# Performance work log

Measured on AMD Instinct MI355X. Metric: run time of the kernel, lower is better.

## Reference

```python
import jax, jax.numpy as jnp
import numpy as np

# Config matching init_kwargs (single TP rank: local heads == total heads)
HID = 1024
NH = 16      # query heads
NKV = 4      # kv heads (GQA)
HD = 64      # head_dim
B = 2
S = 2048
SCALE = 1.0 / HD ** 0.5


def setup_inputs() -> dict:
    key = jax.random.key(0)
    k1, k2, k3 = jax.random.split(key, 3)
    qkv_out = (NH + 2 * NKV) * HD  # 1536
    return {
        "hidden_states": jax.random.normal(k1, (B, S, HID), dtype=jnp.float32),
        "W_qkv": jax.random.normal(k2, (HID, qkv_out), dtype=jnp.float32) * 0.02,
        "W_o": jax.random.normal(k3, (HID, HID), dtype=jnp.float32) * 0.02,
    }


def reference(hidden_states, W_qkv, W_o):
    b, s, _ = hidden_states.shape
    rep = NH // NKV  # GQA repeat factor (repeat_interleave: q head h uses kv group h // rep)

    qkv = hidden_states @ W_qkv  # [B, S, (NH+2*NKV)*HD]
    q, k, v = jnp.split(qkv, [NH * HD, (NH + NKV) * HD], axis=-1)

    # [B, heads, S, HD]
    q = q.reshape(b, s, NH, HD).transpose(0, 2, 1, 3)
    k = k.reshape(b, s, NKV, HD).transpose(0, 2, 1, 3)
    v = v.reshape(b, s, NKV, HD).transpose(0, 2, 1, 3)

    # Group query heads by shared kv head instead of repeat_interleaving K/V in memory.
    qg = q.reshape(b, NKV, rep, s, HD)  # head h = g*rep + r  <=>  kv group g = h // rep
    scores = jnp.einsum("bgrqd,bgkd->bgrqk", qg, k) * SCALE  # [B, NKV, rep, S, S]

    # Causal mask (prefill path: kv_cache is None, seq_len > 1)
    causal = jnp.triu(jnp.ones((s, s), dtype=bool), k=1)
    scores = jnp.where(causal, jnp.finfo(scores.dtype).min, scores)

    attn = jax.nn.softmax(scores, axis=-1)
    out = jnp.einsum("bgrqk,bgkd->bgrqd", attn, v)  # [B, NKV, rep, S, HD]
    out = out.reshape(b, NH, s, HD).transpose(0, 2, 1, 3).reshape(b, s, NH * HD)
    return out @ W_o  # [B, S, HID]
```

## Files before the change

### kernel.cpp

```cpp
#include <hip/hip_runtime.h>
#include <stdint.h>

using u16 = unsigned short;
using u32 = unsigned int;

typedef __attribute__((ext_vector_type(8))) short short8;
typedef __attribute__((ext_vector_type(4))) float f32x4;
typedef __attribute__((ext_vector_type(16))) float f32x16;

__device__ __forceinline__ u16 f2bf(float f) {
  u32 u = __builtin_bit_cast(u32, f);
  u = (u + 0x7fffu + ((u >> 16) & 1u)) >> 16;
  return (u16)u;
}

__device__ __forceinline__ u32 cvtpk(float lo, float hi) {
  u32 r;
  asm("v_cvt_pk_bf16_f32 %0, %1, %2" : "=v"(r) : "v"(lo), "v"(hi));
  return r;
}

__device__ __forceinline__ short8 ld16(const u16* p) {
  uint4 v = *(const uint4*)p;
  union { uint4 u; short8 s; } c; c.u = v; return c.s;
}

__device__ __forceinline__ void gload_lds16(const void* g, void* l) {
  __builtin_amdgcn_global_load_lds(
      (const __attribute__((address_space(1))) void*)g,
      (__attribute__((address_space(3))) void*)l, 16, 0, 0);
}

__device__ __forceinline__ f32x16 mfma32(short8 a, short8 b, f32x16 c) {
  return __builtin_amdgcn_mfma_f32_32x32x16_bf16(a, b, c, 0, 0, 0);
}

__global__ __launch_bounds__(256) void k_prep(const float* __restrict__ hs,
                                              const float* __restrict__ wqkv,
                                              const float* __restrict__ wo,
                                              u16* __restrict__ hsb,
                                              u16* __restrict__ wqkvT,
                                              u16* __restrict__ woT) {
  __shared__ float tile[32][33];
  const int bid = blockIdx.x;
  if (bid < 4096) {
    int i = bid * 256 + threadIdx.x;
    float4 v = ((const float4*)hs)[i];
    ushort4 o;
    o.x = f2bf(v.x); o.y = f2bf(v.y); o.z = f2bf(v.z); o.w = f2bf(v.w);
    ((ushort4*)hsb)[i] = o;
    return;
  }
  const float* in; u16* out; int R, C, bx, by;
  if (bid < 5632) {
    int idx = bid - 4096;
    in = wqkv; out = wqkvT; R = 1024; C = 1536;
    bx = idx % 48; by = idx / 48;
  } else {
    int idx = bid - 5632;
    in = wo; out = woT; R = 1024; C = 1024;
    bx = idx & 31; by = idx >> 5;
  }
  int c0 = bx * 32, r0 = by * 32;
  int tx = threadIdx.x & 31, ty = threadIdx.x >> 5;
#pragma unroll
  for (int i = 0; i < 4; ++i) {
    int r = ty + 8 * i;
    tile[r][tx] = in[(size_t)(r0 + r) * C + c0 + tx];
  }
  __syncthreads();
#pragma unroll
  for (int i = 0; i < 4; ++i) {
    int r = ty + 8 * i;
    out[(size_t)(c0 + r) * R + r0 + tx] = f2bf(tile[tx][r]);
  }
}

__global__ __launch_bounds__(256, 3) void k_gemm_qkv(
    const u16* __restrict__ A, const u16* __restrict__ BT,
    u16* __restrict__ qb, u16* __restrict__ kb, u16* __restrict__ vbT) {
  const int K = 1024;
  __shared__ __align__(16) u16 As[2][64 * 64];
  __shared__ __align__(16) u16 Bs[2][128 * 64];
  const int t = threadIdx.x;
  const int l = t & 63;
  const int wid = t >> 6;
  const int wr = wid >> 1, wc = wid & 1;
  const int lr = l & 15, lg = l >> 4;
  const int cpx = (int)gridDim.x >> 3;
  const int nb = (blockIdx.x & 7) * cpx + ((int)blockIdx.x >> 3);
  const int mt = nb / 12, nt = nb % 12;
  const int m0 = mt << 6, n0 = nt << 7;

  f32x4 zero = {0.f, 0.f, 0.f, 0.f};
  f32x4 acc[2][4];
#pragma unroll
  for (int i = 0; i < 2; ++i)
#pragma unroll
    for (int j = 0; j < 4; ++j) acc[i][j] = zero;

  const u16* Ab = A + (size_t)m0 * K;
  const u16* Bb = BT + (size_t)n0 * K;

  auto STAGE = [&](int kt, int bsel) {
    const u16* Ak = Ab + kt * 64;
    const u16* Bk = Bb + kt * 64;
#pragma unroll
    for (int i = 0; i < 2; ++i) {
      int o16 = i * 256 + t;
      int row = o16 >> 3, c = o16 & 7;
      int sc = c ^ (row & 7);
      gload_lds16(Ak + (size_t)row * K + sc * 8, &As[bsel][o16 * 8]);
    }
#pragma unroll
    for (int i = 0; i < 4; ++i) {
      int o16 = i * 256 + t;
      int row = o16 >> 3, c = o16 & 7;
      int sc = c ^ (row & 7);
      gload_lds16(Bk + (size_t)row * K + sc * 8, &Bs[bsel][o16 * 8]);
    }
  };

  STAGE(0, 0);
  asm volatile("s_waitcnt vmcnt(0)" ::: "memory");
  __builtin_amdgcn_s_barrier();

  for (int kt = 0; kt < 16; ++kt) {
    const int cur = kt & 1;
    if (kt + 1 < 16) STAGE(kt + 1, cur ^ 1);
#pragma unroll
    for (int ks = 0; ks < 2; ++ks) {
      short8 a[2], b[4];
#pragma unroll
      for (int mi = 0; mi < 2; ++mi) {
        int row = wr * 32 + mi * 16 + lr;
        int c = (ks * 4 + lg) ^ (row & 7);
        a[mi] = ld16(&As[cur][(row * 8 + c) * 8]);
      }
#pragma unroll
      for (int ni = 0; ni < 4; ++ni) {
        int row = wc * 64 + ni * 16 + lr;
        int c = (ks * 4 + lg) ^ (row & 7);
        b[ni] = ld16(&Bs[cur][(row * 8 + c) * 8]);
      }
#pragma unroll
      for (int mi = 0; mi < 2; ++mi)
#pragma unroll
        for (int ni = 0; ni < 4; ++ni)
          acc[mi][ni] = __builtin_amdgcn_mfma_f32_16x16x32_bf16(a[mi], b[ni], acc[mi][ni], 0, 0, 0);
    }
    asm volatile("s_waitcnt vmcnt(0)" ::: "memory");
    __builtin_amdgcn_s_barrier();
    asm volatile("" ::: "memory");
  }

#pragma unroll
  for (int mi = 0; mi < 2; ++mi) {
#pragma unroll
    for (int ni = 0; ni < 4; ++ni) {
#pragma unroll
      for (int r = 0; r < 4; ++r) {
        float v = acc[mi][ni][r];
        int m = m0 + wr * 32 + mi * 16 + 4 * lg + r;
        int n = n0 + wc * 64 + ni * 16 + lr;
        int bb = m >> 11, s = m & 2047;
        int tau = s >> 5, i32e = s & 31;
        if (n < 1024) {
          int h = n >> 6, d = n & 63;
          int kc = d >> 4, hi2 = (d >> 3) & 1, e = d & 7;
          qb[((size_t)(bb * 16 + h)) * 131072 +
             (size_t)((tau * 4 + kc) * 64 + (hi2 << 5 | i32e)) * 8 + e] = f2bf(v * 0.18033688f);
        } else if (n < 1280) {
          int g = (n - 1024) >> 6, d = n & 63;
          int kc = d >> 4, hi2 = (d >> 3) & 1, e = d & 7;
          kb[((size_t)(bb * 4 + g)) * 131072 +
             (size_t)((tau * 4 + kc) * 64 + (hi2 << 5 | i32e)) * 8 + e] = f2bf(v);
        } else {
          int g = (n - 1280) >> 6, dT = n & 63;
          int c = (s >> 4) & 1, hi2 = (s >> 3) & 1, e = s & 7;
          int dd = dT >> 5, i32v = dT & 31;
          vbT[((size_t)(bb * 4 + g)) * 131072 +
              (size_t)(((tau * 2 + dd) * 2 + c) * 64 + (hi2 << 5 | i32v)) * 8 + e] = f2bf(v);
        }
      }
    }
  }
}

__global__ __launch_bounds__(256, 2) void k_gemm_out(
    const u16* __restrict__ A, const u16* __restrict__ BT, float* __restrict__ out) {
  const int K = 1024, N = 1024;
  __shared__ __align__(16) u16 As[2][64 * 64];
  __shared__ __align__(16) u16 Bs[2][128 * 64];
  const int t = threadIdx.x;
  const int l = t & 63;
  const int wid = t >> 6;
  const int wr = wid >> 1, wc = wid & 1;
  const int lr = l & 15, lg = l >> 4;
  const int cpx = (int)gridDim.x >> 3;
  const int nb = (blockIdx.x & 7) * cpx + ((int)blockIdx.x >> 3);
  const int mt = nb >> 3, nt = nb & 7;
  const int m0 = mt << 6, n0 = nt << 7;

  f32x4 zero = {0.f, 0.f, 0.f, 0.f};
  f32x4 acc[2][4];
#pragma unroll
  for (int i = 0; i < 2; ++i)
#pragma unroll
    for (int j = 0; j < 4; ++j) acc[i][j] = zero;

  const u16* Ab = A + (size_t)m0 * K;
  const u16* Bb = BT + (size_t)n0 * K;

  auto STAGE = [&](int kt, int bsel) {
    const u16* Ak = Ab + kt * 64;
    const u16* Bk = Bb + kt * 64;
#pragma unroll
    for (int i = 0; i < 2; ++i) {
      int o16 = i * 256 + t;
      int row = o16 >> 3, c = o16 & 7;
      int sc = c ^ (row & 7);
      gload_lds16(Ak + (size_t)row * K + sc * 8, &As[bsel][o16 * 8]);
    }
#pragma unroll
    for (int i = 0; i < 4; ++i) {
      int o16 = i * 256 + t;
      int row = o16 >> 3, c = o16 & 7;
      int sc = c ^ (row & 7);
      gload_lds16(Bk + (size_t)row * K + sc * 8, &Bs[bsel][o16 * 8]);
    }
  };

  STAGE(0, 0);
  asm volatile("s_waitcnt vmcnt(0)" ::: "memory");
  __builtin_amdgcn_s_barrier();

  for (int kt = 0; kt < 16; ++kt) {
    const int cur = kt & 1;
    if (kt + 1 < 16) STAGE(kt + 1, cur ^ 1);
#pragma unroll
    for (int ks = 0; ks < 2; ++ks) {
      short8 a[2], b[4];
#pragma unroll
      for (int mi = 0; mi < 2; ++mi) {
        int row = wr * 32 + mi * 16 + lr;
        int c = (ks * 4 + lg) ^ (row & 7);
        a[mi] = ld16(&As[cur][(row * 8 + c) * 8]);
      }
#pragma unroll
      for (int ni = 0; ni < 4; ++ni) {
        int row = wc * 64 + ni * 16 + lr;
        int c = (ks * 4 + lg) ^ (row & 7);
        b[ni] = ld16(&Bs[cur][(row * 8 + c) * 8]);
      }
#pragma unroll
      for (int mi = 0; mi < 2; ++mi)
#pragma unroll
        for (int ni = 0; ni < 4; ++ni)
          acc[mi][ni] = __builtin_amdgcn_mfma_f32_16x16x32_bf16(a[mi], b[ni], acc[mi][ni], 0, 0, 0);
    }
    asm volatile("s_waitcnt vmcnt(0)" ::: "memory");
    __builtin_amdgcn_s_barrier();
    asm volatile("" ::: "memory");
  }

#pragma unroll
  for (int mi = 0; mi < 2; ++mi)
#pragma unroll
    for (int ni = 0; ni < 4; ++ni)
#pragma unroll
      for (int r = 0; r < 4; ++r) {
        int m = m0 + wr * 32 + mi * 16 + 4 * lg + r;
        int n = n0 + wc * 64 + ni * 16 + lr;
        out[(size_t)m * N + n] = acc[mi][ni][r];
      }
}

__global__ __launch_bounds__(256, 1) void k_attn(const u16* __restrict__ qbuf,
                                                 const u16* __restrict__ kbuf,
                                                 const u16* __restrict__ vbuf,
                                                 u16* __restrict__ attn) {
  __shared__ float osh[2][4096];
  __shared__ float lsh[2][128];
  const int t = threadIdx.x;
  const int l = t & 63, wid = t >> 6;
  const int i32 = l & 31, hi = l >> 5;
  const int bh = blockIdx.x >> 3;
  const int jj = blockIdx.x & 7;
  const int b = bh >> 4, h = bh & 15, g = h >> 2;
  const int slot = wid >> 1, w01 = wid & 1;
  const int cc = jj + slot * 8;
  const int pA = cc, pB = 31 - cc;
  const int split = 16 - cc;

  const u16* qp = qbuf + ((size_t)(b * 16 + h)) * 131072;
  const u16* kp = kbuf + ((size_t)(b * 4 + g)) * 131072;
  const u16* vp = vbuf + ((size_t)(b * 4 + g)) * 131072;

  f32x16 z16 = {0.f, 0.f, 0.f, 0.f, 0.f, 0.f, 0.f, 0.f,
                0.f, 0.f, 0.f, 0.f, 0.f, 0.f, 0.f, 0.f};
  short8 qfa[4], qfb[4];
  f32x16 oa[2], ob[2];
  float la, lb;
  short8 kA[2][4], kB[2][4];

  auto LOADQ = [&](int p) {
#pragma unroll
    for (int kc = 0; kc < 4; ++kc) {
      qfa[kc] = ld16(qp + ((size_t)((2 * p) * 4 + kc) * 64 + l) * 8);
      qfb[kc] = ld16(qp + ((size_t)((2 * p + 1) * 4 + kc) * 64 + l) * 8);
    }
  };

  auto LOADK = [&](short8(&kf)[2][4], int kv0) {
#pragma unroll
    for (int mf = 0; mf < 2; ++mf)
#pragma unroll
      for (int kc = 0; kc < 4; ++kc)
        kf[mf][kc] = ld16(kp + ((size_t)((((kv0 >> 5) + mf) * 4 + kc)) * 64 + l) * 8);
  };

  auto SOFTPV = [&](f32x16(&sc)[2], short8(&vf)[2][2][2], f32x16(&o)[2], float& ls,
                    bool dmask, int ilocb) {
    if (dmask) {
#pragma unroll
      for (int mf = 0; mf < 2; ++mf)
#pragma unroll
        for (int R = 0; R < 16; ++R) {
          int j2 = 32 * mf + (R & 3) + 8 * (R >> 2) + 4 * hi;
          if (j2 > ilocb + i32) sc[mf][R] = -1e30f;
        }
    }
    float s0 = 0.f, s1 = 0.f, s2 = 0.f, s3 = 0.f;
#pragma unroll
    for (int mf = 0; mf < 2; ++mf)
#pragma unroll
      for (int R = 0; R < 16; R += 4) {
        float p0 = __builtin_amdgcn_exp2f(sc[mf][R]);
        float p1 = __builtin_amdgcn_exp2f(sc[mf][R + 1]);
        float p2 = __builtin_amdgcn_exp2f(sc[mf][R + 2]);
        float p3 = __builtin_amdgcn_exp2f(sc[mf][R + 3]);
        sc[mf][R] = p0; sc[mf][R + 1] = p1; sc[mf][R + 2] = p2; sc[mf][R + 3] = p3;
        s0 += p0; s1 += p1; s2 += p2; s3 += p3;
      }
    ls += (s0 + s1) + (s2 + s3);
    short8 pb[2][2];
#pragma unroll
    for (int mf = 0; mf < 2; ++mf)
#pragma unroll
      for (int c = 0; c < 2; ++c) {
        union { u32 w[4]; short8 s8; } U;
#pragma unroll
        for (int q = 0; q < 2; ++q) {
          u32 wa = cvtpk(sc[mf][8 * c + 2 * q], sc[mf][8 * c + 2 * q + 1]);
          u32 wb = cvtpk(sc[mf][8 * c + 4 + 2 * q], sc[mf][8 * c + 4 + 2 * q + 1]);
          auto rr = __builtin_amdgcn_permlane32_swap(wa, wb, false, false);
          U.w[q] = (u32)rr[0];
          U.w[2 + q] = (u32)rr[1];
        }
        pb[mf][c] = U.s8;
      }
    __builtin_amdgcn_s_setprio(1);
#pragma unroll
    for (int mf = 0; mf < 2; ++mf)
#pragma unroll
      for (int c = 0; c < 2; ++c) {
        o[0] = mfma32(vf[0][mf][c], pb[mf][c], o[0]);
        o[1] = mfma32(vf[1][mf][c], pb[mf][c], o[1]);
      }
    __builtin_amdgcn_s_setprio(0);
  };

  auto PROCESS = [&](short8(&kf)[2][4], short8(&kn)[2][4], bool pref, int n, int p) {
    const int kv0 = n * 64;
    short8 vf[2][2][2];
#pragma unroll
    for (int mf = 0; mf < 2; ++mf)
#pragma unroll
      for (int dd = 0; dd < 2; ++dd)
#pragma unroll
        for (int c = 0; c < 2; ++c)
          vf[dd][mf][c] = ld16(vp + ((size_t)((((kv0 >> 5) + mf) * 2 + dd) * 2 + c) * 64 + l) * 8);

    const bool dmask = (n == p);

    f32x16 sc[2];
    __builtin_amdgcn_s_setprio(1);
    sc[0] = mfma32(kf[0][0], qfa[0], z16);
    sc[1] = mfma32(kf[1][0], qfa[0], z16);
#pragma unroll
    for (int kc = 1; kc < 4; ++kc) {
      sc[0] = mfma32(kf[0][kc], qfa[kc], sc[0]);
      sc[1] = mfma32(kf[1][kc], qfa[kc], sc[1]);
    }
    __builtin_amdgcn_s_setprio(0);
    if (pref) LOADK(kn, kv0 + 64);
    SOFTPV(sc, vf, oa, la, dmask, 0);

    f32x16 sd[2];
    __builtin_amdgcn_s_setprio(1);
    sd[0] = mfma32(kf[0][0], qfb[0], z16);
    sd[1] = mfma32(kf[1][0], qfb[0], z16);
#pragma unroll
    for (int kc = 1; kc < 4; ++kc) {
      sd[0] = mfma32(kf[0][kc], qfb[kc], sd[0]);
      sd[1] = mfma32(kf[1][kc], qfb[kc], sd[1]);
    }
    __builtin_amdgcn_s_setprio(0);
    SOFTPV(sd, vf, ob, lb, dmask, 32);
  };

  auto RUN = [&](int p, int n0, int n1) {
    if (n0 >= n1) return;
    LOADQ(p);
    LOADK(kA, n0 * 64);
    int n = n0;
    while (true) {
      PROCESS(kA, kB, n + 1 < n1, n, p);
      if (++n >= n1) break;
      PROCESS(kB, kA, n + 1 < n1, n, p);
      if (++n >= n1) break;
    }
  };

  auto STOREPAIR = [&](int p) {
#pragma unroll
    for (int po = 0; po < 2; ++po) {
      float ls = (po == 0) ? la : lb;
      f32x16* o = (po == 0) ? oa : ob;
      float tot;
      {
        u32 su = __builtin_bit_cast(u32, ls);
        auto rr = __builtin_amdgcn_permlane32_swap(su, su, false, false);
        tot = __builtin_bit_cast(float, (u32)rr[0]) + __builtin_bit_cast(float, (u32)rr[1]);
      }
      float inv = 1.f / tot;
      u16* ao = attn + ((size_t)(b * 2048 + (2 * p + po) * 32)) * 1024 + h * 64;
#pragma unroll
      for (int dd = 0; dd < 2; ++dd) {
#pragma unroll
        for (int R = 0; R < 16; R += 2) {
          int d = dd * 32 + (R & 3) + 8 * (R >> 2) + 4 * hi;
          u32 w = cvtpk(o[dd][R] * inv, o[dd][R + 1] * inv);
          *(u32*)(ao + (size_t)i32 * 1024 + d) = w;
        }
      }
    }
  };

  oa[0] = z16; oa[1] = z16; ob[0] = z16; ob[1] = z16; la = 0.f; lb = 0.f;
  if (w01 == 0) {
    RUN(pA, 0, pA + 1);
    STOREPAIR(pA);
    oa[0] = z16; oa[1] = z16; ob[0] = z16; ob[1] = z16; la = 0.f; lb = 0.f;
    RUN(pB, 0, split);
    float* dst = &osh[slot][0];
#pragma unroll
    for (int po = 0; po < 2; ++po) {
      f32x16* o = (po == 0) ? oa : ob;
#pragma unroll
      for (int dd = 0; dd < 2; ++dd) {
        float4* d4 = (float4*)&dst[((po * 2 + dd) * 64 + l) * 16];
#pragma unroll
        for (int q = 0; q < 4; ++q) {
          float4 v4;
          v4.x = o[dd][4 * q]; v4.y = o[dd][4 * q + 1];
          v4.z = o[dd][4 * q + 2]; v4.w = o[dd][4 * q + 3];
          d4[q] = v4;
        }
      }
    }
    lsh[slot][l] = la;
    lsh[slot][64 + l] = lb;
  } else {
    RUN(pB, split, pB + 1);
  }
  __syncthreads();
  if (w01 == 1) {
    const float* src = &osh[slot][0];
#pragma unroll
    for (int po = 0; po < 2; ++po) {
      f32x16* o = (po == 0) ? oa : ob;
#pragma unroll
      for (int dd = 0; dd < 2; ++dd) {
        const float4* s4 = (const float4*)&src[((po * 2 + dd) * 64 + l) * 16];
#pragma unroll
        for (int q = 0; q < 4; ++q) {
          float4 v4 = s4[q];
          o[dd][4 * q] += v4.x; o[dd][4 * q + 1] += v4.y;
          o[dd][4 * q + 2] += v4.z; o[dd][4 * q + 3] += v4.w;
        }
      }
    }
    la += lsh[slot][l];
    lb += lsh[slot][64 + l];
    STOREPAIR(pB);
  }
}

extern "C" void kernel_launch(void* const* d_in, const int* in_sizes, int n_in,
                              void* d_out, int out_size, void* d_ws, size_t ws_size,
                              hipStream_t stream) {
  const float* hs = (const float*)d_in[0];
  const float* wqkv = (const float*)d_in[1];
  const float* wo = (const float*)d_in[2];
  float* out = (float*)d_out;
  u16* ws = (u16*)d_ws;

  u16* hsb = ws;
  u16* wqkvT = hsb + 4194304;
  u16* woT = wqkvT + 1572864;
  u16* qb = woT + 1048576;
  u16* kb = qb + 4194304;
  u16* vb = kb + 1048576;
  u16* attn = vb + 1048576;
  (void)in_sizes; (void)n_in; (void)out_size; (void)ws_size;

  k_prep<<<6656, 256, 0, stream>>>(hs, wqkv, wo, hsb, wqkvT, woT);
  k_gemm_qkv<<<768, 256, 0, stream>>>(hsb, wqkvT, qb, kb, vb);
  k_attn<<<256, 256, 0, stream>>>(qb, kb, vb, attn);
  k_gemm_out<<<512, 256, 0, stream>>>(attn, woT, out);
}
```

Before: 84.17 us.

## Fuse hidden_states fp32-to-bf16 conversion into QKV GEMM A-tile loads

Drops the separate pass that turned hidden_states into bf16 in the prep kernel. The QKV GEMM now reads fp32 A tiles straight into registers, converts them with v_cvt_pk_bf16_f32, and writes them into swizzled LDS after the MFMA phase. This removes a full 16 MB read plus 8 MB write round trip through the workspace. In exchange each A tile (64 rows) is read twice as many bytes by 12 N-tile blocks, and the asynchronous LDS loads become register-staged loads.

```diff
diff --git a/kernel.cpp b/kernel.cpp
--- a/kernel.cpp
+++ b/kernel.cpp
@@ -35,29 +35,18 @@
   return __builtin_amdgcn_mfma_f32_32x32x16_bf16(a, b, c, 0, 0, 0);
 }
 
-__global__ __launch_bounds__(256) void k_prep(const float* __restrict__ hs,
-                                              const float* __restrict__ wqkv,
+__global__ __launch_bounds__(256) void k_prep(const float* __restrict__ wqkv,
                                               const float* __restrict__ wo,
-                                              u16* __restrict__ hsb,
                                               u16* __restrict__ wqkvT,
                                               u16* __restrict__ woT) {
   __shared__ float tile[32][33];
   const int bid = blockIdx.x;
-  if (bid < 4096) {
-    int i = bid * 256 + threadIdx.x;
-    float4 v = ((const float4*)hs)[i];
-    ushort4 o;
-    o.x = f2bf(v.x); o.y = f2bf(v.y); o.z = f2bf(v.z); o.w = f2bf(v.w);
-    ((ushort4*)hsb)[i] = o;
-    return;
-  }
   const float* in; u16* out; int R, C, bx, by;
-  if (bid < 5632) {
-    int idx = bid - 4096;
+  if (bid < 1536) {
     in = wqkv; out = wqkvT; R = 1024; C = 1536;
-    bx = idx % 48; by = idx / 48;
+    bx = bid % 48; by = bid / 48;
   } else {
-    int idx = bid - 5632;
+    int idx = bid - 1536;
     in = wo; out = woT; R = 1024; C = 1024;
     bx = idx & 31; by = idx >> 5;
   }
@@ -77,7 +66,7 @@
 }
 
 __global__ __launch_bounds__(256, 3) void k_gemm_qkv(
-    const u16* __restrict__ A, const u16* __restrict__ BT,
+    const float* __restrict__ hsF, const u16* __restrict__ BT,
     u16* __restrict__ qb, u16* __restrict__ kb, u16* __restrict__ vbT) {
   const int K = 1024;
   __shared__ __align__(16) u16 As[2][64 * 64];
@@ -99,19 +88,31 @@
 #pragma unroll
     for (int j = 0; j < 4; ++j) acc[i][j] = zero;
 
-  const u16* Ab = A + (size_t)m0 * K;
+  const float* Ab = hsF + (size_t)m0 * K;
   const u16* Bb = BT + (size_t)n0 * K;
 
-  auto STAGE = [&](int kt, int bsel) {
-    const u16* Ak = Ab + kt * 64;
+  auto LOADA = [&](int kt, float4(&ar)[4]) {
+#pragma unroll
+    for (int i = 0; i < 4; ++i) {
+      int idx = i * 256 + t;
+      int row = idx >> 4, h2 = idx & 15;
+      ar[i] = *(const float4*)(Ab + (size_t)row * K + kt * 64 + h2 * 4);
+    }
+  };
+  auto WRITEA = [&](int bsel, float4(&ar)[4]) {
+#pragma unroll
+    for (int i = 0; i < 4; ++i) {
+      int idx = i * 256 + t;
+      int row = idx >> 4, h2 = idx & 15;
+      int c = h2 >> 1, half = h2 & 1;
+      u32 w0 = cvtpk(ar[i].x, ar[i].y);
+      u32 w1 = cvtpk(ar[i].z, ar[i].w);
+      u32* dst = (u32*)&As[bsel][(row * 8 + (c ^ (row & 7))) * 8 + half * 4];
+      dst[0] = w0; dst[1] = w1;
+    }
+  };
+  auto STAGEB = [&](int kt, int bsel) {
     const u16* Bk = Bb + kt * 64;
-#pragma unroll
-    for (int i = 0; i < 2; ++i) {
-      int o16 = i * 256 + t;
-      int row = o16 >> 3, c = o16 & 7;
-      int sc = c ^ (row & 7);
-      gload_lds16(Ak + (size_t)row * K + sc * 8, &As[bsel][o16 * 8]);
-    }
 #pragma unroll
     for (int i = 0; i < 4; ++i) {
       int o16 = i * 256 + t;
@@ -121,13 +122,22 @@
     }
   };
 
-  STAGE(0, 0);
-  asm volatile("s_waitcnt vmcnt(0)" ::: "memory");
+  {
+    float4 ar[4];
+    LOADA(0, ar);
+    STAGEB(0, 0);
+    WRITEA(0, ar);
+  }
+  asm volatile("s_waitcnt vmcnt(0) lgkmcnt(0)" ::: "memory");
   __builtin_amdgcn_s_barrier();
 
   for (int kt = 0; kt < 16; ++kt) {
     const int cur = kt & 1;
-    if (kt + 1 < 16) STAGE(kt + 1, cur ^ 1);
+    float4 ar[4];
+    if (kt + 1 < 16) {
+      LOADA(kt + 1, ar);
+      STAGEB(kt + 1, cur ^ 1);
+    }
 #pragma unroll
     for (int ks = 0; ks < 2; ++ks) {
       short8 a[2], b[4];
@@ -149,7 +159,8 @@
         for (int ni = 0; ni < 4; ++ni)
           acc[mi][ni] = __builtin_amdgcn_mfma_f32_16x16x32_bf16(a[mi], b[ni], acc[mi][ni], 0, 0, 0);
     }
-    asm volatile("s_waitcnt vmcnt(0)" ::: "memory");
+    if (kt + 1 < 16) WRITEA(cur ^ 1, ar);
+    asm volatile("s_waitcnt vmcnt(0) lgkmcnt(0)" ::: "memory");
     __builtin_amdgcn_s_barrier();
     asm volatile("" ::: "memory");
   }
@@ -507,8 +518,7 @@
   float* out = (float*)d_out;
   u16* ws = (u16*)d_ws;
 
-  u16* hsb = ws;
-  u16* wqkvT = hsb + 4194304;
+  u16* wqkvT = ws;
   u16* woT = wqkvT + 1572864;
   u16* qb = woT + 1048576;
   u16* kb = qb + 4194304;
@@ -516,8 +526,8 @@
   u16* attn = vb + 1048576;
   (void)in_sizes; (void)n_in; (void)out_size; (void)ws_size;
 
-  k_prep<<<6656, 256, 0, stream>>>(hs, wqkv, wo, hsb, wqkvT, woT);
-  k_gemm_qkv<<<768, 256, 0, stream>>>(hsb, wqkvT, qb, kb, vb);
+  k_prep<<<2560, 256, 0, stream>>>(wqkv, wo, wqkvT, woT);
+  k_gemm_qkv<<<768, 256, 0, stream>>>(hs, wqkvT, qb, kb, vb);
   k_attn<<<256, 256, 0, stream>>>(qb, kb, vb, attn);
   k_gemm_out<<<512, 256, 0, stream>>>(attn, woT, out);
 }
```

Result: slower. 86.86 us (+3.2%).

## Triple-buffer LDS in QKV and output GEMMs with two-stage-ahead prefetch

Applied to the files above, without the earlier changes.

Both projection GEMMs switch from double to triple-buffered LDS staging. Tiles are prefetched two k-steps ahead, with a partial vmcnt wait and a single barrier per iteration instead of a full drain at the end of each step. The goal is to hide global-to-LDS latency behind MFMA work. In exchange, LDS use grows by half and the QKV kernel's occupancy bound drops from 3 to 2 blocks per CU.

```diff
diff --git a/kernel.cpp b/kernel.cpp
--- a/kernel.cpp
+++ b/kernel.cpp
@@ -76,12 +76,12 @@
   }
 }
 
-__global__ __launch_bounds__(256, 3) void k_gemm_qkv(
+__global__ __launch_bounds__(256, 2) void k_gemm_qkv(
     const u16* __restrict__ A, const u16* __restrict__ BT,
     u16* __restrict__ qb, u16* __restrict__ kb, u16* __restrict__ vbT) {
   const int K = 1024;
-  __shared__ __align__(16) u16 As[2][64 * 64];
-  __shared__ __align__(16) u16 Bs[2][128 * 64];
+  __shared__ __align__(16) u16 As[3][64 * 64];
+  __shared__ __align__(16) u16 Bs[3][128 * 64];
   const int t = threadIdx.x;
   const int l = t & 63;
   const int wid = t >> 6;
@@ -122,12 +122,17 @@
   };
 
   STAGE(0, 0);
-  asm volatile("s_waitcnt vmcnt(0)" ::: "memory");
-  __builtin_amdgcn_s_barrier();
-
+  STAGE(1, 1);
+
+  int cur = 0;
   for (int kt = 0; kt < 16; ++kt) {
-    const int cur = kt & 1;
-    if (kt + 1 < 16) STAGE(kt + 1, cur ^ 1);
+    if (kt + 1 < 16) { asm volatile("s_waitcnt vmcnt(6)" ::: "memory"); }
+    else             { asm volatile("s_waitcnt vmcnt(0)" ::: "memory"); }
+    __builtin_amdgcn_s_barrier();
+    if (kt + 2 < 16) {
+      int nxt2 = cur - 1 < 0 ? 2 : cur - 1;
+      STAGE(kt + 2, nxt2);
+    }
 #pragma unroll
     for (int ks = 0; ks < 2; ++ks) {
       short8 a[2], b[4];
@@ -149,9 +154,7 @@
         for (int ni = 0; ni < 4; ++ni)
           acc[mi][ni] = __builtin_amdgcn_mfma_f32_16x16x32_bf16(a[mi], b[ni], acc[mi][ni], 0, 0, 0);
     }
-    asm volatile("s_waitcnt vmcnt(0)" ::: "memory");
-    __builtin_amdgcn_s_barrier();
-    asm volatile("" ::: "memory");
+    cur = cur + 1 == 3 ? 0 : cur + 1;
   }
 
 #pragma unroll
@@ -190,8 +193,8 @@
 __global__ __launch_bounds__(256, 2) void k_gemm_out(
     const u16* __restrict__ A, const u16* __restrict__ BT, float* __restrict__ out) {
   const int K = 1024, N = 1024;
-  __shared__ __align__(16) u16 As[2][64 * 64];
-  __shared__ __align__(16) u16 Bs[2][128 * 64];
+  __shared__ __align__(16) u16 As[3][64 * 64];
+  __shared__ __align__(16) u16 Bs[3][128 * 64];
   const int t = threadIdx.x;
   const int l = t & 63;
   const int wid = t >> 6;
@@ -232,12 +235,17 @@
   };
 
   STAGE(0, 0);
-  asm volatile("s_waitcnt vmcnt(0)" ::: "memory");
-  __builtin_amdgcn_s_barrier();
-
+  STAGE(1, 1);
+
+  int cur = 0;
   for (int kt = 0; kt < 16; ++kt) {
-    const int cur = kt & 1;
-    if (kt + 1 < 16) STAGE(kt + 1, cur ^ 1);
+    if (kt + 1 < 16) { asm volatile("s_waitcnt vmcnt(6)" ::: "memory"); }
+    else             { asm volatile("s_waitcnt vmcnt(0)" ::: "memory"); }
+    __builtin_amdgcn_s_barrier();
+    if (kt + 2 < 16) {
+      int nxt2 = cur - 1 < 0 ? 2 : cur - 1;
+      STAGE(kt + 2, nxt2);
+    }
 #pragma unroll
     for (int ks = 0; ks < 2; ++ks) {
       short8 a[2], b[4];
@@ -259,9 +267,7 @@
         for (int ni = 0; ni < 4; ++ni)
           acc[mi][ni] = __builtin_amdgcn_mfma_f32_16x16x32_bf16(a[mi], b[ni], acc[mi][ni], 0, 0, 0);
     }
-    asm volatile("s_waitcnt vmcnt(0)" ::: "memory");
-    __builtin_amdgcn_s_barrier();
-    asm volatile("" ::: "memory");
+    cur = cur + 1 == 3 ? 0 : cur + 1;
   }
 
 #pragma unroll
```

Result: slower. 89.79 us (+6.7%).
